# Kernel tuning notes

Hardware: AMD Instinct MI355X
Metric: run time of the kernel (lower is better)

The kernel has to match this reference:

```python
import jax, jax.numpy as jnp
import numpy as np

NUM_RATIOS = 3  # len(anchor_ratios)
FPN_C = 256
SHARED_C = 512
LEVEL_SIZES = [256, 128, 64, 32, 16]
BATCH = 2


def _conv2d(x, w, b, padding):
    # x: [B,H,W,Cin], w: [kh,kw,Cin,Cout]
    y = jax.lax.conv_general_dilated(
        x, w, window_strides=(1, 1), padding=padding,
        dimension_numbers=('NHWC', 'HWIO', 'NHWC'))
    return y + b


def setup_inputs() -> dict:
    key = jax.random.key(0)
    ks = jax.random.split(key, 16)
    inp = {}
    for i, s in enumerate(LEVEL_SIZES):
        inp[f'feat_p{i+2}'] = jax.random.normal(ks[i], (BATCH, s, s, FPN_C), dtype=jnp.float32)
    # He-normal initialized conv params
    def he(k, shape):
        fan_in = shape[0] * shape[1] * shape[2]
        return jax.random.normal(k, shape, dtype=jnp.float32) * np.sqrt(2.0 / fan_in).astype(np.float32)
    inp['w_shared'] = he(ks[5], (3, 3, FPN_C, SHARED_C))
    inp['b_shared'] = jnp.zeros((SHARED_C,), jnp.float32)
    inp['w_cls'] = he(ks[6], (1, 1, SHARED_C, NUM_RATIOS * 2))
    inp['b_cls'] = jnp.zeros((NUM_RATIOS * 2,), jnp.float32)
    inp['w_delta'] = he(ks[7], (1, 1, SHARED_C, NUM_RATIOS * 4))
    inp['b_delta'] = jnp.zeros((NUM_RATIOS * 4,), jnp.float32)
    return inp


def reference(feat_p2, feat_p3, feat_p4, feat_p5, feat_p6,
              w_shared, b_shared, w_cls, b_cls, w_delta, b_delta):
    feats = [feat_p2, feat_p3, feat_p4, feat_p5, feat_p6]
    logits_l, probs_l, deltas_l = [], [], []
    for feat in feats:
        B = feat.shape[0]
        shared = jax.nn.relu(_conv2d(feat, w_shared, b_shared, 'SAME'))
        x = _conv2d(shared, w_cls, b_cls, 'VALID')          # [B,H,W,2*R]
        rpn_class_logits = x.reshape(B, -1, 2)              # [B, H*W*R, 2]
        rpn_probs = jax.nn.softmax(rpn_class_logits, axis=-1)
        x = _conv2d(shared, w_delta, b_delta, 'VALID')      # [B,H,W,4*R]
        rpn_deltas = x.reshape(B, -1, 4)                    # [B, H*W*R, 4]
        logits_l.append(rpn_class_logits)
        probs_l.append(rpn_probs)
        deltas_l.append(rpn_deltas)
    rpn_class_logits = jnp.concatenate(logits_l, axis=1)
    rpn_probs = jnp.concatenate(probs_l, axis=1)
    rpn_deltas = jnp.concatenate(deltas_l, axis=1)
    return (rpn_class_logits, rpn_probs, rpn_deltas)
```

## Files before the change

kernel.cpp:

```cpp
#include <hip/hip_runtime.h>

typedef unsigned short u16;
typedef unsigned int u32;
typedef __attribute__((ext_vector_type(8))) short bf16x8;
typedef __attribute__((ext_vector_type(4))) float f32x4;

#define TR 261888
#define LOGITS_OFF 0
#define PROBS_OFF  1047552
#define DELTAS_OFF 2095104

#define W3P_ELEMS (72 * 512 * 32)
#define W18P_ELEMS (32 * 512)
#define FLAG_OFF_BYTES ((W3P_ELEMS + W18P_ELEMS) * 2)

__device__ __forceinline__ float b2f(u16 u) {
    union { u32 i; float f; } v; v.i = ((u32)u) << 16; return v.f;
}
__device__ __forceinline__ u16 f2b(float f) {
    union { float f; u32 i; } v; v.f = f;
    u32 x = v.i;
    return (u16)((x + 0x7fffu + ((x >> 16) & 1u)) >> 16);
}
__device__ __forceinline__ float ldmix(const void* p, int i, bool isb16) {
    return isb16 ? b2f(((const u16*)p)[i]) : ((const float*)p)[i];
}

__device__ __forceinline__ int sh_idx(int px, int c) {
    return px * 512 + (c ^ ((px & 3) * 8));
}

__global__ void detect_kernel(const u16* __restrict__ f0, int* __restrict__ flag) {
    int lane = threadIdx.x;
    u16 v = f0[lane * 2];
    int e = (v >> 7) & 0xFF;
    bool plausible = (e >= 90) && (e <= 140);
    unsigned long long m = __ballot(plausible);
    if (lane == 0) *flag = (__popcll(m) >= 48) ? 1 : 0;
}

__global__ void repack_kernel(const void* __restrict__ w3,
                              const void* __restrict__ wcls,
                              const void* __restrict__ wdelta,
                              u16* __restrict__ W3p, u16* __restrict__ W18p,
                              const int* __restrict__ flag) {
    const bool isb16 = (*flag != 0);
    int tid = blockIdx.x * 256 + threadIdx.x;
    if (tid < W3P_ELEMS) {
        int k = tid & 31;
        int n = (tid >> 5) & 511;
        int c = tid >> 14;
        int K = c * 32 + k;
        float v = ldmix(w3, K * 512 + n, isb16);
        W3p[tid] = f2b(v);
    } else if (tid < W3P_ELEMS + W18P_ELEMS) {
        int t = tid - W3P_ELEMS;
        int k = t & 511;
        int j = t >> 9;
        float v = 0.f;
        if (j < 6)       v = ldmix(wcls, k * 6 + j, isb16);
        else if (j < 18) v = ldmix(wdelta, k * 12 + (j - 6), isb16);
        W18p[t] = f2b(v);
    }
}

__global__ __launch_bounds__(256, 2) void rpn_main(
    const void* __restrict__ f0, const void* __restrict__ f1,
    const void* __restrict__ f2, const void* __restrict__ f3,
    const void* __restrict__ f4,
    const void* __restrict__ bsh, const void* __restrict__ bcls,
    const void* __restrict__ bdelta,
    const u16* __restrict__ W3p, const u16* __restrict__ W18p,
    void* __restrict__ out, const int* __restrict__ flag)
{
    __shared__ u16 SMEM[32768];

    const bool isb16 = (*flag != 0);

    const int tid  = threadIdx.x;
    const int wv   = tid >> 6;
    const int lane = tid & 63;
    const int quad = lane >> 4;
    const int l16  = lane & 15;

    const int bid = blockIdx.x;
    const int lvl = (bid >= 2048) + (bid >= 2560) + (bid >= 2688) + (bid >= 2720);
    const int tileBase = (lvl == 0) ? 0 : (lvl == 1) ? 2048 : (lvl == 2) ? 2560
                        : (lvl == 3) ? 2688 : 2720;
    const int logS   = 8 - lvl;
    const int S      = 1 << logS;
    const int rowOff = (lvl == 0) ? 0 : (lvl == 1) ? 196608 : (lvl == 2) ? 245760
                      : (lvl == 3) ? 258048 : 261120;
    const void* feat = (lvl == 0) ? f0 : (lvl == 1) ? f1 : (lvl == 2) ? f2
                      : (lvl == 3) ? f3 : f4;
    const int tile = bid - tileBase;

    const int logT = logS - 3;
    const int b    = tile >> (2 * logT);
    const int t2   = tile & ((1 << (2 * logT)) - 1);
    const int th   = t2 >> logT;
    const int tw   = t2 & ((1 << logT) - 1);
    const int h0   = th << 3, w0 = tw << 3;

    for (int g = tid; g < 3200; g += 256) {
        const int p  = g >> 5;
        const int cg = g & 31;
        const int hh = p / 10;
        const int ww = p - hh * 10;
        const int ih = h0 + hh - 1;
        const int iw = w0 + ww - 1;
        uint4 v; v.x = 0u; v.y = 0u; v.z = 0u; v.w = 0u;
        if (ih >= 0 && ih < S && iw >= 0 && iw < S) {
            const size_t gaddr = ((size_t)((b * S + ih) * S + iw)) * 256 + cg * 8;
            if (isb16) {
                v = *(const uint4*)((const u16*)feat + gaddr);
            } else {
                const float* fp = (const float*)feat + gaddr;
                float4 x = *(const float4*)fp;
                float4 y = *(const float4*)(fp + 4);
                v.x = (u32)f2b(x.x) | ((u32)f2b(x.y) << 16);
                v.y = (u32)f2b(x.z) | ((u32)f2b(x.w) << 16);
                v.z = (u32)f2b(y.x) | ((u32)f2b(y.y) << 16);
                v.w = (u32)f2b(y.z) | ((u32)f2b(y.w) << 16);
            }
        }
        *(uint4*)&SMEM[p * 256 + ((cg ^ (p & 7)) << 3)] = v;
    }
    __syncthreads();

    const f32x4 zf = {0.f, 0.f, 0.f, 0.f};
    f32x4 acc[4][8];
#pragma unroll
    for (int mt = 0; mt < 4; ++mt)
#pragma unroll
        for (int nt = 0; nt < 8; ++nt) acc[mt][nt] = zf;

    const int pLane0 = ((l16 >> 3) + 1) * 10 + (l16 & 7) + 1;
    const int wbase  = (wv * 128 + l16) * 32 + quad * 8;

    for (int tap = 0; tap < 9; ++tap) {
        const int dh = tap / 3 - 1, dw = tap % 3 - 1;
        int sbase[4], sx[4];
#pragma unroll
        for (int mt = 0; mt < 4; ++mt) {
            const int p = pLane0 + (mt * 2 + dh) * 10 + dw;
            sbase[mt] = p * 256;
            sx[mt]    = p & 7;
        }
        const u16* Wk = &W3p[tap * 8 * 16384 + wbase];
#pragma unroll
        for (int cc = 0; cc < 8; ++cc) {
            bf16x8 bfr[8];
#pragma unroll
            for (int nt = 0; nt < 8; ++nt)
                bfr[nt] = *(const bf16x8*)&Wk[cc * 16384 + nt * 512];
#pragma unroll
            for (int mt = 0; mt < 4; ++mt) {
                const bf16x8 af = *(const bf16x8*)
                    &SMEM[sbase[mt] + (((cc * 4 + quad) ^ sx[mt]) << 3)];
#pragma unroll
                for (int nt = 0; nt < 8; ++nt)
                    acc[mt][nt] = __builtin_amdgcn_mfma_f32_16x16x32_bf16(
                        af, bfr[nt], acc[mt][nt], 0, 0, 0);
            }
        }
    }

    __syncthreads();

#pragma unroll
    for (int nt = 0; nt < 8; ++nt) {
        const int n = wv * 128 + nt * 16 + l16;
        const float bn = ldmix(bsh, n, isb16);
#pragma unroll
        for (int mt = 0; mt < 4; ++mt) {
#pragma unroll
            for (int r = 0; r < 4; ++r) {
                const int px = mt * 16 + quad * 4 + r;
                float vv = acc[mt][nt][r] + bn;
                vv = vv > 0.f ? vv : 0.f;
                SMEM[sh_idx(px, n)] = f2b(vv);
            }
        }
    }
    __syncthreads();

    f32x4 a2[2];
    a2[0] = zf; a2[1] = zf;
#pragma unroll
    for (int jt = 0; jt < 2; ++jt) {
#pragma unroll
        for (int ks = 0; ks < 16; ++ks) {
            bf16x8 wa = *(const bf16x8*)&W18p[(jt * 16 + l16) * 512 + ks * 32 + quad * 8];
            bf16x8 sb = *(const bf16x8*)&SMEM[sh_idx(wv * 16 + l16, ks * 32 + quad * 8)];
            a2[jt] = __builtin_amdgcn_mfma_f32_16x16x32_bf16(wa, sb, a2[jt], 0, 0, 0);
        }
    }

    const int px2  = wv * 16 + l16;
    const int Pimg = (h0 + (px2 >> 3)) * S + (w0 + (px2 & 7));
    const size_t rowBase = (size_t)b * TR + rowOff + (size_t)Pimg * 3;
    u16*   o16 = (u16*)out;
    float* o32 = (float*)out;
    auto storeOut = [&](size_t idx, float v) {
        if (isb16) o16[idx] = f2b(v); else o32[idx] = v;
    };

#pragma unroll
    for (int jt = 0; jt < 2; ++jt) {
#pragma unroll
        for (int r = 0; r < 4; ++r) {
            const int j = jt * 16 + quad * 4 + r;
            if (j >= 6 && j < 18) {
                const int dj = j - 6;
                float vv = a2[jt][r] + ldmix(bdelta, dj, isb16);
                storeOut(DELTAS_OFF + (rowBase + (dj >> 2)) * 4 + (dj & 3), vv);
            }
        }
    }
    auto writePair = [&](int r, float v0, float v1) {
        const float bl0 = ldmix(bcls, 2 * r, isb16);
        const float bl1 = ldmix(bcls, 2 * r + 1, isb16);
        const float L0 = v0 + bl0, L1 = v1 + bl1;
        const size_t row = rowBase + r;
        storeOut(LOGITS_OFF + row * 2 + 0, L0);
        storeOut(LOGITS_OFF + row * 2 + 1, L1);
        const float m = fmaxf(L0, L1);
        const float e0 = __expf(L0 - m), e1 = __expf(L1 - m);
        const float inv = 1.0f / (e0 + e1);
        storeOut(PROBS_OFF + row * 2 + 0, e0 * inv);
        storeOut(PROBS_OFF + row * 2 + 1, e1 * inv);
    };
    if (quad == 0) {
        writePair(0, a2[0][0], a2[0][1]);
        writePair(1, a2[0][2], a2[0][3]);
    } else if (quad == 1) {
        writePair(2, a2[0][0], a2[0][1]);
    }
}

extern "C" void kernel_launch(void* const* d_in, const int* in_sizes, int n_in,
                              void* d_out, int out_size, void* d_ws, size_t ws_size,
                              hipStream_t stream) {
    const void* f0     = d_in[0];
    const void* f1     = d_in[1];
    const void* f2     = d_in[2];
    const void* f3     = d_in[3];
    const void* f4     = d_in[4];
    const void* w3     = d_in[5];
    const void* bsh    = d_in[6];
    const void* wcls   = d_in[7];
    const void* bcls   = d_in[8];
    const void* wdelta = d_in[9];
    const void* bdelta = d_in[10];

    u16* W3p  = (u16*)d_ws;
    u16* W18p = W3p + W3P_ELEMS;
    int* flag = (int*)((char*)d_ws + FLAG_OFF_BYTES);

    detect_kernel<<<1, 64, 0, stream>>>((const u16*)f0, flag);
    repack_kernel<<<4672, 256, 0, stream>>>(w3, wcls, wdelta, W3p, W18p, flag);
    rpn_main<<<2728, 256, 0, stream>>>(f0, f1, f2, f3, f4,
                                       bsh, bcls, bdelta, W3p, W18p,
                                       d_out, flag);
}
```

Baseline: 703.2 us.

## Split conv output channels across two blocks and finalize heads separately

```diff
diff --git a/kernel.cpp b/kernel.cpp
--- a/kernel.cpp
+++ b/kernel.cpp
@@ -13,6 +13,10 @@
 #define W3P_ELEMS (72 * 512 * 32)
 #define W18P_ELEMS (32 * 512)
 #define FLAG_OFF_BYTES ((W3P_ELEMS + W18P_ELEMS) * 2)
+#define PART0_OFF 2392320
+#define NPIX 174592
+#define PART_ELEMS (NPIX * 18)
+#define PART_BYTES (PART_ELEMS * 4)
 
 __device__ __forceinline__ float b2f(u16 u) {
     union { u32 i; float f; } v; v.i = ((u32)u) << 16; return v.f;
@@ -64,16 +68,15 @@
     }
 }
 
-__global__ __launch_bounds__(256, 2) void rpn_main(
+__global__ __launch_bounds__(256, 3) void rpn_conv(
     const void* __restrict__ f0, const void* __restrict__ f1,
     const void* __restrict__ f2, const void* __restrict__ f3,
     const void* __restrict__ f4,
-    const void* __restrict__ bsh, const void* __restrict__ bcls,
-    const void* __restrict__ bdelta,
+    const void* __restrict__ bsh,
     const u16* __restrict__ W3p, const u16* __restrict__ W18p,
-    void* __restrict__ out, const int* __restrict__ flag)
+    float* __restrict__ Ppart, const int* __restrict__ flag)
 {
-    __shared__ u16 SMEM[32768];
+    __shared__ u16 SMEM[25600];
 
     const bool isb16 = (*flag != 0);
 
@@ -83,17 +86,20 @@
     const int quad = lane >> 4;
     const int l16  = lane & 15;
 
-    const int bid = blockIdx.x;
-    const int lvl = (bid >= 2048) + (bid >= 2560) + (bid >= 2688) + (bid >= 2720);
+    const int gid    = blockIdx.x;
+    const int tileId = gid >> 1;
+    const int nhalf  = gid & 1;
+
+    const int lvl = (tileId >= 2048) + (tileId >= 2560) + (tileId >= 2688) + (tileId >= 2720);
     const int tileBase = (lvl == 0) ? 0 : (lvl == 1) ? 2048 : (lvl == 2) ? 2560
                         : (lvl == 3) ? 2688 : 2720;
     const int logS   = 8 - lvl;
     const int S      = 1 << logS;
-    const int rowOff = (lvl == 0) ? 0 : (lvl == 1) ? 196608 : (lvl == 2) ? 245760
-                      : (lvl == 3) ? 258048 : 261120;
+    const int lvlPixOff = (lvl == 0) ? 0 : (lvl == 1) ? 65536 : (lvl == 2) ? 81920
+                         : (lvl == 3) ? 86016 : 87040;
     const void* feat = (lvl == 0) ? f0 : (lvl == 1) ? f1 : (lvl == 2) ? f2
                       : (lvl == 3) ? f3 : f4;
-    const int tile = bid - tileBase;
+    const int tile = tileId - tileBase;
 
     const int logT = logS - 3;
     const int b    = tile >> (2 * logT);
@@ -129,6 +135,212 @@
     __syncthreads();
 
     const f32x4 zf = {0.f, 0.f, 0.f, 0.f};
+    f32x4 acc[4][4];
+#pragma unroll
+    for (int mt = 0; mt < 4; ++mt)
+#pragma unroll
+        for (int nt = 0; nt < 4; ++nt) acc[mt][nt] = zf;
+
+    const int pLane0 = ((l16 >> 3) + 1) * 10 + (l16 & 7) + 1;
+    const u32 wbase = (u32)(nhalf * 256 + wv * 64 + l16) * 32 + (u32)quad * 8;
+    const u16* __restrict__ Wp = W3p + wbase;
+
+    bf16x8 wA[4], wB[4];
+#pragma unroll
+    for (int nt = 0; nt < 4; ++nt) wA[nt] = *(const bf16x8*)&Wp[nt * 512];
+
+    for (int tap = 0; tap < 9; ++tap) {
+        const int dh = tap / 3 - 1, dw = tap % 3 - 1;
+        int sbase[4], sx[4];
+#pragma unroll
+        for (int mt = 0; mt < 4; ++mt) {
+            const int p = pLane0 + (mt * 2 + dh) * 10 + dw;
+            sbase[mt] = p * 256;
+            sx[mt]    = p & 7;
+        }
+#pragma unroll
+        for (int cc = 0; cc < 8; cc += 2) {
+            const int kc = tap * 8 + cc;
+#pragma unroll
+            for (int nt = 0; nt < 4; ++nt)
+                wB[nt] = *(const bf16x8*)&Wp[(kc + 1) * 16384 + nt * 512];
+            bf16x8 af[4];
+#pragma unroll
+            for (int mt = 0; mt < 4; ++mt)
+                af[mt] = *(const bf16x8*)
+                    &SMEM[sbase[mt] + (((cc * 4 + quad) ^ sx[mt]) << 3)];
+#pragma unroll
+            for (int mt = 0; mt < 4; ++mt)
+#pragma unroll
+                for (int nt = 0; nt < 4; ++nt)
+                    acc[mt][nt] = __builtin_amdgcn_mfma_f32_16x16x32_bf16(
+                        af[mt], wA[nt], acc[mt][nt], 0, 0, 0);
+            if (kc + 2 < 72) {
+#pragma unroll
+                for (int nt = 0; nt < 4; ++nt)
+                    wA[nt] = *(const bf16x8*)&Wp[(kc + 2) * 16384 + nt * 512];
+            }
+            bf16x8 ag[4];
+#pragma unroll
+            for (int mt = 0; mt < 4; ++mt)
+                ag[mt] = *(const bf16x8*)
+                    &SMEM[sbase[mt] + ((((cc + 1) * 4 + quad) ^ sx[mt]) << 3)];
+#pragma unroll
+            for (int mt = 0; mt < 4; ++mt)
+#pragma unroll
+                for (int nt = 0; nt < 4; ++nt)
+                    acc[mt][nt] = __builtin_amdgcn_mfma_f32_16x16x32_bf16(
+                        ag[mt], wB[nt], acc[mt][nt], 0, 0, 0);
+        }
+    }
+
+    __syncthreads();
+
+#pragma unroll
+    for (int nt = 0; nt < 4; ++nt) {
+        const int nl = wv * 64 + nt * 16 + l16;
+        const float bn = ldmix(bsh, nhalf * 256 + nl, isb16);
+#pragma unroll
+        for (int mt = 0; mt < 4; ++mt) {
+#pragma unroll
+            for (int r = 0; r < 4; ++r) {
+                const int px = mt * 16 + quad * 4 + r;
+                float vv = acc[mt][nt][r] + bn;
+                vv = vv > 0.f ? vv : 0.f;
+                SMEM[px * 256 + (nl ^ ((px & 7) * 8))] = f2b(vv);
+            }
+        }
+    }
+    __syncthreads();
+
+    f32x4 a2[2];
+    a2[0] = zf; a2[1] = zf;
+    const int px2 = wv * 16 + l16;
+#pragma unroll
+    for (int jt = 0; jt < 2; ++jt) {
+#pragma unroll
+        for (int ksl = 0; ksl < 8; ++ksl) {
+            bf16x8 wa = *(const bf16x8*)
+                &W18p[(jt * 16 + l16) * 512 + nhalf * 256 + ksl * 32 + quad * 8];
+            bf16x8 sb = *(const bf16x8*)
+                &SMEM[px2 * 256 + ((ksl * 32 + quad * 8) ^ ((px2 & 7) * 8))];
+            a2[jt] = __builtin_amdgcn_mfma_f32_16x16x32_bf16(wa, sb, a2[jt], 0, 0, 0);
+        }
+    }
+
+    const int Pimg = (h0 + (px2 >> 3)) * S + (w0 + (px2 & 7));
+    const int pixG = b * 87296 + lvlPixOff + Pimg;
+    float* P = Ppart + (size_t)nhalf * PART_ELEMS + (size_t)pixG * 18;
+    *(f32x4*)&P[quad * 4] = a2[0];
+    if (quad == 0) { P[16] = a2[1][0]; P[17] = a2[1][1]; }
+}
+
+__global__ __launch_bounds__(256) void rpn_finalize(
+    const float* __restrict__ P0, const float* __restrict__ P1,
+    const void* __restrict__ bcls, const void* __restrict__ bdelta,
+    void* __restrict__ out, const int* __restrict__ flag)
+{
+    const bool isb16 = (*flag != 0);
+    const int pixG = blockIdx.x * 256 + threadIdx.x;
+    if (pixG >= NPIX) return;
+
+    float v[18];
+#pragma unroll
+    for (int j = 0; j < 18; ++j)
+        v[j] = P0[(size_t)pixG * 18 + j] + P1[(size_t)pixG * 18 + j];
+
+    const size_t rowBase = (size_t)pixG * 3;
+    u16*   o16 = (u16*)out;
+    float* o32 = (float*)out;
+    auto storeOut = [&](size_t idx, float val) {
+        if (isb16) o16[idx] = f2b(val); else o32[idx] = val;
+    };
+
+#pragma unroll
+    for (int dj = 0; dj < 12; ++dj) {
+        float vv = v[6 + dj] + ldmix(bdelta, dj, isb16);
+        storeOut(DELTAS_OFF + (rowBase + (dj >> 2)) * 4 + (dj & 3), vv);
+    }
+#pragma unroll
+    for (int r = 0; r < 3; ++r) {
+        const float L0 = v[2 * r]     + ldmix(bcls, 2 * r, isb16);
+        const float L1 = v[2 * r + 1] + ldmix(bcls, 2 * r + 1, isb16);
+        const size_t row = rowBase + r;
+        storeOut(LOGITS_OFF + row * 2 + 0, L0);
+        storeOut(LOGITS_OFF + row * 2 + 1, L1);
+        const float m = fmaxf(L0, L1);
+        const float e0 = __expf(L0 - m), e1 = __expf(L1 - m);
+        const float inv = 1.0f / (e0 + e1);
+        storeOut(PROBS_OFF + row * 2 + 0, e0 * inv);
+        storeOut(PROBS_OFF + row * 2 + 1, e1 * inv);
+    }
+}
+
+__global__ __launch_bounds__(256, 2) void rpn_fused(
+    const void* __restrict__ f0, const void* __restrict__ f1,
+    const void* __restrict__ f2, const void* __restrict__ f3,
+    const void* __restrict__ f4,
+    const void* __restrict__ bsh, const void* __restrict__ bcls,
+    const void* __restrict__ bdelta,
+    const u16* __restrict__ W3p, const u16* __restrict__ W18p,
+    void* __restrict__ out, const int* __restrict__ flag)
+{
+    __shared__ u16 SMEM[32768];
+
+    const bool isb16 = (*flag != 0);
+
+    const int tid  = threadIdx.x;
+    const int wv   = tid >> 6;
+    const int lane = tid & 63;
+    const int quad = lane >> 4;
+    const int l16  = lane & 15;
+
+    const int bid = blockIdx.x;
+    const int lvl = (bid >= 2048) + (bid >= 2560) + (bid >= 2688) + (bid >= 2720);
+    const int tileBase = (lvl == 0) ? 0 : (lvl == 1) ? 2048 : (lvl == 2) ? 2560
+                        : (lvl == 3) ? 2688 : 2720;
+    const int logS   = 8 - lvl;
+    const int S      = 1 << logS;
+    const int rowOff = (lvl == 0) ? 0 : (lvl == 1) ? 196608 : (lvl == 2) ? 245760
+                      : (lvl == 3) ? 258048 : 261120;
+    const void* feat = (lvl == 0) ? f0 : (lvl == 1) ? f1 : (lvl == 2) ? f2
+                      : (lvl == 3) ? f3 : f4;
+    const int tile = bid - tileBase;
+
+    const int logT = logS - 3;
+    const int b    = tile >> (2 * logT);
+    const int t2   = tile & ((1 << (2 * logT)) - 1);
+    const int th   = t2 >> logT;
+    const int tw   = t2 & ((1 << logT) - 1);
+    const int h0   = th << 3, w0 = tw << 3;
+
+    for (int g = tid; g < 3200; g += 256) {
+        const int p  = g >> 5;
+        const int cg = g & 31;
+        const int hh = p / 10;
+        const int ww = p - hh * 10;
+        const int ih = h0 + hh - 1;
+        const int iw = w0 + ww - 1;
+        uint4 v; v.x = 0u; v.y = 0u; v.z = 0u; v.w = 0u;
+        if (ih >= 0 && ih < S && iw >= 0 && iw < S) {
+            const size_t gaddr = ((size_t)((b * S + ih) * S + iw)) * 256 + cg * 8;
+            if (isb16) {
+                v = *(const uint4*)((const u16*)feat + gaddr);
+            } else {
+                const float* fp = (const float*)feat + gaddr;
+                float4 x = *(const float4*)fp;
+                float4 y = *(const float4*)(fp + 4);
+                v.x = (u32)f2b(x.x) | ((u32)f2b(x.y) << 16);
+                v.y = (u32)f2b(x.z) | ((u32)f2b(x.w) << 16);
+                v.z = (u32)f2b(y.x) | ((u32)f2b(y.y) << 16);
+                v.w = (u32)f2b(y.z) | ((u32)f2b(y.w) << 16);
+            }
+        }
+        *(uint4*)&SMEM[p * 256 + ((cg ^ (p & 7)) << 3)] = v;
+    }
+    __syncthreads();
+
+    const f32x4 zf = {0.f, 0.f, 0.f, 0.f};
     f32x4 acc[4][8];
 #pragma unroll
     for (int mt = 0; mt < 4; ++mt)
@@ -260,7 +472,17 @@
 
     detect_kernel<<<1, 64, 0, stream>>>((const u16*)f0, flag);
     repack_kernel<<<4672, 256, 0, stream>>>(w3, wcls, wdelta, W3p, W18p, flag);
-    rpn_main<<<2728, 256, 0, stream>>>(f0, f1, f2, f3, f4,
-                                       bsh, bcls, bdelta, W3p, W18p,
-                                       d_out, flag);
-}
+
+    const size_t NEED = (size_t)PART0_OFF + 2ull * PART_BYTES;
+    if (ws_size >= NEED) {
+        float* P0 = (float*)((char*)d_ws + PART0_OFF);
+        float* P1 = P0 + PART_ELEMS;
+        rpn_conv<<<5456, 256, 0, stream>>>(f0, f1, f2, f3, f4, bsh,
+                                           W3p, W18p, P0, flag);
+        rpn_finalize<<<682, 256, 0, stream>>>(P0, P1, bcls, bdelta, d_out, flag);
+    } else {
+        rpn_fused<<<2728, 256, 0, stream>>>(f0, f1, f2, f3, f4,
+                                            bsh, bcls, bdelta, W3p, W18p,
+                                            d_out, flag);
+    }
+}
```

Measured after the change: 683.6 us. 1.03x faster.

## Switch 3x3 conv main loop to 32x32x16 MFMA with prefetched weights

Applied to the files above, without the earlier changes.

```diff
diff --git a/kernel.cpp b/kernel.cpp
--- a/kernel.cpp
+++ b/kernel.cpp
@@ -4,6 +4,7 @@
 typedef unsigned int u32;
 typedef __attribute__((ext_vector_type(8))) short bf16x8;
 typedef __attribute__((ext_vector_type(4))) float f32x4;
+typedef __attribute__((ext_vector_type(16))) float f32x16;
 
 #define TR 261888
 #define LOGITS_OFF 0
@@ -80,6 +81,8 @@
     const int tid  = threadIdx.x;
     const int wv   = tid >> 6;
     const int lane = tid & 63;
+    const int l32  = lane & 31;
+    const int hi   = lane >> 5;
     const int quad = lane >> 4;
     const int l16  = lane & 15;
 
@@ -124,59 +127,80 @@
                 v.w = (u32)f2b(y.z) | ((u32)f2b(y.w) << 16);
             }
         }
-        *(uint4*)&SMEM[p * 256 + ((cg ^ (p & 7)) << 3)] = v;
+        const int sw = (p & 7) | ((hh & 1) << 3);
+        *(uint4*)&SMEM[p * 256 + ((cg ^ sw) << 3)] = v;
     }
     __syncthreads();
 
-    const f32x4 zf = {0.f, 0.f, 0.f, 0.f};
-    f32x4 acc[4][8];
-#pragma unroll
-    for (int mt = 0; mt < 4; ++mt)
-#pragma unroll
-        for (int nt = 0; nt < 8; ++nt) acc[mt][nt] = zf;
-
-    const int pLane0 = ((l16 >> 3) + 1) * 10 + (l16 & 7) + 1;
-    const int wbase  = (wv * 128 + l16) * 32 + quad * 8;
+    f32x16 acc[2][4];
+#pragma unroll
+    for (int mt = 0; mt < 2; ++mt)
+#pragma unroll
+        for (int nt = 0; nt < 4; ++nt)
+#pragma unroll
+            for (int r = 0; r < 16; ++r) acc[mt][nt][r] = 0.f;
+
+    const int pLane32 = ((l32 >> 3) + 1) * 10 + (l32 & 7) + 1;
+    const u16* __restrict__ Wp = W3p + (u32)(wv * 128 + l32) * 32 + (u32)hi * 8;
+
+    bf16x8 wq[8];
+#pragma unroll
+    for (int i = 0; i < 8; ++i)
+        wq[i] = *(const bf16x8*)&Wp[(i >> 1) * 1024 + (i & 1) * 16];
+
+#define CHUNK(CC)                                                             \
+    {                                                                         \
+        const int kc = tap * 8 + (CC);                                        \
+        const int kcn = (kc + 1 < 72) ? (kc + 1) : kc;                        \
+        bf16x8 af[2][2];                                                      \
+        _Pragma("unroll")                                                     \
+        for (int mt = 0; mt < 2; ++mt)                                        \
+            _Pragma("unroll")                                                 \
+            for (int ks = 0; ks < 2; ++ks)                                    \
+                af[mt][ks] = *(const bf16x8*)                                 \
+                    &SMEM[sbase[mt] +                                         \
+                          ((((CC) * 4 + ks * 2 + hi) ^ sx[mt]) << 3)];        \
+        __builtin_amdgcn_s_setprio(1);                                        \
+        _Pragma("unroll")                                                     \
+        for (int ks = 0; ks < 2; ++ks)                                        \
+            _Pragma("unroll")                                                 \
+            for (int nt = 0; nt < 4; ++nt) {                                  \
+                acc[0][nt] = __builtin_amdgcn_mfma_f32_32x32x16_bf16(         \
+                    af[0][ks], wq[nt * 2 + ks], acc[0][nt], 0, 0, 0);         \
+                acc[1][nt] = __builtin_amdgcn_mfma_f32_32x32x16_bf16(         \
+                    af[1][ks], wq[nt * 2 + ks], acc[1][nt], 0, 0, 0);         \
+                wq[nt * 2 + ks] = *(const bf16x8*)                            \
+                    &Wp[(size_t)kcn * 16384 + nt * 1024 + ks * 16];           \
+            }                                                                 \
+        __builtin_amdgcn_s_setprio(0);                                        \
+    }
 
     for (int tap = 0; tap < 9; ++tap) {
         const int dh = tap / 3 - 1, dw = tap % 3 - 1;
-        int sbase[4], sx[4];
-#pragma unroll
-        for (int mt = 0; mt < 4; ++mt) {
-            const int p = pLane0 + (mt * 2 + dh) * 10 + dw;
+        const int rowpar = ((l32 >> 3) + 1 + dh) & 1;
+        int sbase[2], sx[2];
+#pragma unroll
+        for (int mt = 0; mt < 2; ++mt) {
+            const int p = pLane32 + (mt * 4 + dh) * 10 + dw;
             sbase[mt] = p * 256;
-            sx[mt]    = p & 7;
-        }
-        const u16* Wk = &W3p[tap * 8 * 16384 + wbase];
-#pragma unroll
-        for (int cc = 0; cc < 8; ++cc) {
-            bf16x8 bfr[8];
-#pragma unroll
-            for (int nt = 0; nt < 8; ++nt)
-                bfr[nt] = *(const bf16x8*)&Wk[cc * 16384 + nt * 512];
-#pragma unroll
-            for (int mt = 0; mt < 4; ++mt) {
-                const bf16x8 af = *(const bf16x8*)
-                    &SMEM[sbase[mt] + (((cc * 4 + quad) ^ sx[mt]) << 3)];
-#pragma unroll
-                for (int nt = 0; nt < 8; ++nt)
-                    acc[mt][nt] = __builtin_amdgcn_mfma_f32_16x16x32_bf16(
-                        af, bfr[nt], acc[mt][nt], 0, 0, 0);
-            }
-        }
-    }
+            sx[mt]    = (p & 7) | (rowpar << 3);
+        }
+        CHUNK(0) CHUNK(1) CHUNK(2) CHUNK(3)
+        CHUNK(4) CHUNK(5) CHUNK(6) CHUNK(7)
+    }
+#undef CHUNK
 
     __syncthreads();
 
 #pragma unroll
-    for (int nt = 0; nt < 8; ++nt) {
-        const int n = wv * 128 + nt * 16 + l16;
+    for (int nt = 0; nt < 4; ++nt) {
+        const int n = wv * 128 + nt * 32 + l32;
         const float bn = ldmix(bsh, n, isb16);
 #pragma unroll
-        for (int mt = 0; mt < 4; ++mt) {
-#pragma unroll
-            for (int r = 0; r < 4; ++r) {
-                const int px = mt * 16 + quad * 4 + r;
+        for (int mt = 0; mt < 2; ++mt) {
+#pragma unroll
+            for (int r = 0; r < 16; ++r) {
+                const int px = mt * 32 + (r & 3) + 8 * (r >> 2) + 4 * hi;
                 float vv = acc[mt][nt][r] + bn;
                 vv = vv > 0.f ? vv : 0.f;
                 SMEM[sh_idx(px, n)] = f2b(vv);
@@ -185,6 +209,7 @@
     }
     __syncthreads();
 
+    const f32x4 zf = {0.f, 0.f, 0.f, 0.f};
     f32x4 a2[2];
     a2[0] = zf; a2[1] = zf;
 #pragma unroll
```

Result: faster. 688.8 us (-2.0%).
